# Performance work log

Measured on AMD Instinct MI355X. Metric: run time of the kernel, lower is better.

The kernel has to match this reference:

```python
import jax, jax.numpy as jnp
import numpy as np

VOCAB, HID, L, HEADS, INTER, MAXSEQ, NCLS = 30522, 128, 2, 2, 512, 512, 2
HEAD = HID // HEADS
B, S = 128, 512


def _tlin(x, W, b):
    # TernaryLinear: threshold-quantize W to {-1,0,1} with per-tensor scale,
    # then ordinary linear. delta = 0.7*mean|W|, alpha = mean|W| over kept entries.
    absW = jnp.abs(W)
    delta = 0.7 * jnp.mean(absW)
    mask = (absW > delta).astype(W.dtype)
    alpha = jnp.sum(absW * mask) / jnp.maximum(jnp.sum(mask), 1.0)
    Wq = jnp.sign(W) * mask * alpha  # [out, in]
    return jnp.einsum('...i,oi->...o', x, Wq) + b


def _ln(x, g, b, eps=1e-5):
    m = jnp.mean(x, axis=-1, keepdims=True)
    v = jnp.var(x, axis=-1, keepdims=True)
    return (x - m) * jax.lax.rsqrt(v + eps) * g + b


def setup_inputs() -> dict:
    key = jax.random.key(0)
    ks = iter(jax.random.split(key, 64))
    n = lambda shape, s=0.02: jax.random.normal(next(ks), shape, dtype=jnp.float32) * s
    inp = {
        'input_ids': jax.random.randint(next(ks), (B, S), 0, VOCAB, dtype=jnp.int32).astype(jnp.int64),
        'tok_emb': n((VOCAB, HID)),
        'pos_emb': n((MAXSEQ, HID)),
        'ln_g': jnp.ones((HID,), jnp.float32), 'ln_b': jnp.zeros((HID,), jnp.float32),
        'qw': n((L, HID, HID)), 'qb': jnp.zeros((L, HID), jnp.float32),
        'kw': n((L, HID, HID)), 'kb': jnp.zeros((L, HID), jnp.float32),
        'vw': n((L, HID, HID)), 'vb': jnp.zeros((L, HID), jnp.float32),
        'aow': n((L, HID, HID)), 'aob': jnp.zeros((L, HID), jnp.float32),
        'iw': n((L, INTER, HID)), 'ib': jnp.zeros((L, INTER), jnp.float32),
        'fow': n((L, HID, INTER)), 'fob': jnp.zeros((L, HID), jnp.float32),
        'ln1g': jnp.ones((L, HID), jnp.float32), 'ln1b': jnp.zeros((L, HID), jnp.float32),
        'ln2g': jnp.ones((L, HID), jnp.float32), 'ln2b': jnp.zeros((L, HID), jnp.float32),
        'clf_w': n((NCLS, HID)), 'clf_b': jnp.zeros((NCLS,), jnp.float32),
    }
    return inp


def reference(input_ids, tok_emb, pos_emb, ln_g, ln_b, qw, qb, kw, kb, vw, vb,
              aow, aob, iw, ib, fow, fob, ln1g, ln1b, ln2g, ln2b, clf_w, clf_b):
    b, s = input_ids.shape
    x = tok_emb[input_ids] + pos_emb[jnp.arange(s)][None, :, :]  # [B,S,H]
    x = _ln(x, ln_g, ln_b)
    scale = 1.0 / (HEAD ** 0.5)
    for l in range(L):
        q = _tlin(x, qw[l], qb[l]).reshape(b, s, HEADS, HEAD)
        k = _tlin(x, kw[l], kb[l]).reshape(b, s, HEADS, HEAD)
        v = _tlin(x, vw[l], vb[l]).reshape(b, s, HEADS, HEAD)
        scores = jnp.einsum('bqhd,bkhd->bhqk', q, k) * scale
        attn = jax.nn.softmax(scores, axis=-1)
        ctx = jnp.einsum('bhqk,bkhd->bqhd', attn, v).reshape(b, s, HID)
        attn_out = _tlin(ctx, aow[l], aob[l])
        x = _ln(x + attn_out, ln1g[l], ln1b[l])
        ff = _tlin(jax.nn.relu(_tlin(x, iw[l], ib[l])), fow[l], fob[l])
        x = _ln(x + ff, ln2g[l], ln2b[l])
    cls = x[:, 0, :]
    logits = _tlin(cls, clf_w, clf_b)  # [B, NCLS]
    return logits
```

## Files before the change

kernel.cpp:

```cpp
#include <hip/hip_runtime.h>

typedef short bf8s __attribute__((ext_vector_type(8)));
typedef float f32x4 __attribute__((ext_vector_type(4)));

#define MFMA16(a, b, c) __builtin_amdgcn_mfma_f32_16x16x32_bf16(a, b, c, 0, 0, 0)

constexpr int S_ = 512, HID_ = 128, B_ = 128, M_ = B_ * S_;

__device__ inline short f2bf(float f) {
  unsigned u = __float_as_uint(f);
  u = (u + 0x7fffu + ((u >> 16) & 1u)) >> 16;
  return (short)u;
}
__device__ inline float bf2f(short s) {
  return __uint_as_float(((unsigned)(unsigned short)s) << 16);
}

__device__ __forceinline__ void async16(void* lds, const void* g) {
  __builtin_amdgcn_global_load_lds(
      (const __attribute__((address_space(1))) unsigned int*)g,
      (__attribute__((address_space(3))) unsigned int*)lds, 16, 0, 0);
}

__device__ __forceinline__ bf8s ldsb(const short* base, int byteoff) {
  return *(const bf8s*)((const char*)base + byteoff);
}

__device__ inline float block_red1024(float v, float* red) {
  #pragma unroll
  for (int m = 32; m >= 1; m >>= 1) v += __shfl_xor(v, m);
  __syncthreads();
  if ((threadIdx.x & 63) == 0) red[threadIdx.x >> 6] = v;
  __syncthreads();
  float t = 0.f;
  #pragma unroll
  for (int i = 0; i < 16; ++i) t += red[i];
  return t;
}

__device__ inline void mat_info(int mat, const float* qw, const float* kw,
                                const float* vw, const float* aow, const float* iw,
                                const float* fw, const float* cw,
                                const float** src, int* n, int* doff, int* lc) {
  if (mat < 6) {
    int l = mat / 3, which = mat % 3;
    const float* t[3] = {qw, kw, vw};
    *src = t[which] + l * 16384; *n = 16384; *doff = l * 49152 + which * 16384;
    *lc = 7;
  } else if (mat < 8) {
    int l = mat - 6;
    *src = aow + l * 16384; *n = 16384; *doff = 98304 + l * 16384; *lc = 7;
  } else if (mat < 10) {
    *src = iw + (mat - 8) * 65536; *n = 65536; *doff = 131072 + (mat - 8) * 65536;
    *lc = 7;
  } else if (mat < 12) {
    *src = fw + (mat - 10) * 65536; *n = 65536; *doff = 262144 + (mat - 10) * 65536;
    *lc = 9;
  } else {
    *src = cw; *n = 256; *doff = 393216; *lc = 0;
  }
}

__global__ __launch_bounds__(1024) void k_qe(const float* qw, const float* kw,
    const float* vw, const float* aow, const float* iw, const float* fw,
    const float* cw, short* WQ,
    const int* __restrict__ ids, const float* __restrict__ tok,
    const float* __restrict__ pos, const float* __restrict__ g,
    const float* __restrict__ bb, short* xb) {
  __shared__ float red[16];
  int tid = threadIdx.x;
  if (blockIdx.x < 13) {
    const float* src; int n, doff, lc;
    mat_info(blockIdx.x, qw, kw, vw, aow, iw, fw, cw, &src, &n, &doff, &lc);
    float s = 0.f;
    for (int i = tid; i < n; i += 1024) s += fabsf(src[i]);
    s = block_red1024(s, red);
    float delta = 0.7f * s / (float)n;
    float s2 = 0.f, c2 = 0.f;
    for (int i = tid; i < n; i += 1024) {
      float a = fabsf(src[i]);
      if (a > delta) { s2 += a; c2 += 1.f; }
    }
    s2 = block_red1024(s2, red);
    c2 = block_red1024(c2, red);
    float alpha = s2 / fmaxf(c2, 1.f);
    if (lc) {
      int nf8 = n >> 3;
      for (int fo8 = tid; fo8 < nf8; fo8 += 1024) {
        int fo = fo8 << 3;
        int tile = fo >> (lc + 4);
        int rem = fo & ((16 << lc) - 1);
        int kblk = rem >> 9;
        int rem2 = rem & 511;
        int sub = rem2 >> 7;
        int r16 = (rem2 >> 3) & 15;
        int r = (tile << 4) | r16;
        int cbase = (kblk << 5) | (sub << 3);
        const float* sp = src + ((size_t)r << lc) + cbase;
        float4 w0 = *(const float4*)(sp);
        float4 w1 = *(const float4*)(sp + 4);
        float wv[8] = {w0.x, w0.y, w0.z, w0.w, w1.x, w1.y, w1.z, w1.w};
        bf8s q;
        #pragma unroll
        for (int j = 0; j < 8; ++j) {
          float w = wv[j];
          q[j] = (fabsf(w) > delta) ? f2bf(w > 0.f ? alpha : -alpha) : (short)0;
        }
        *(bf8s*)(WQ + doff + fo) = q;
      }
    } else {
      for (int i = tid; i < n; i += 1024) {
        float w = src[i];
        WQ[doff + i] = (fabsf(w) > delta) ? f2bf(w > 0.f ? alpha : -alpha) : (short)0;
      }
    }
  } else {
    int wave = tid >> 6, lane = tid & 63;
    int half = lane >> 5, l32 = lane & 31;
    int t = (blockIdx.x - 13) * 32 + wave * 2 + half;
    int s = t & (S_ - 1);
    int id = ids[t];
    int d0 = l32 * 4;
    float4 te = *(const float4*)(tok + (size_t)id * HID_ + d0);
    float4 pe = *(const float4*)(pos + (size_t)s * HID_ + d0);
    float e0 = te.x + pe.x, e1 = te.y + pe.y, e2 = te.z + pe.z, e3 = te.w + pe.w;
    float sum = e0 + e1 + e2 + e3;
    float ssq = e0 * e0 + e1 * e1 + e2 * e2 + e3 * e3;
    #pragma unroll
    for (int m = 16; m >= 1; m >>= 1) {
      sum += __shfl_xor(sum, m);
      ssq += __shfl_xor(ssq, m);
    }
    float mean = sum / 128.f;
    float var = ssq / 128.f - mean * mean;
    float rs = rsqrtf(var + 1e-5f);
    float4 g4 = *(const float4*)(g + d0);
    float4 b4 = *(const float4*)(bb + d0);
    short4 o;
    o.x = f2bf((e0 - mean) * rs * g4.x + b4.x);
    o.y = f2bf((e1 - mean) * rs * g4.y + b4.y);
    o.z = f2bf((e2 - mean) * rs * g4.z + b4.z);
    o.w = f2bf((e3 - mean) * rs * g4.w + b4.w);
    *(short4*)(xb + (size_t)t * HID_ + d0) = o;
  }
}

__global__ __launch_bounds__(256) void k_qkv(
    const short* __restrict__ A, const short* __restrict__ W,
    const float* __restrict__ b0, const float* __restrict__ b1,
    const float* __restrict__ b2, short* outb) {
  __shared__ short Wl[16384];
  int tid = threadIdx.x, lane = tid & 63, wave = tid >> 6;
  int row16 = lane & 15, quad = lane >> 4;
  int tok0 = blockIdx.x * 64 + wave * 16;

  const char* Wm = (const char*)W + blockIdx.y * 32768;
  #pragma unroll
  for (int t = 0; t < 8; ++t)
    async16((char*)Wl + t * 4096 + wave * 1024,
            Wm + t * 4096 + wave * 1024 + lane * 16);

  const short* arow = A + (size_t)(tok0 + row16) * 128 + quad * 8;
  bf8s av[4];
  #pragma unroll
  for (int ki = 0; ki < 4; ++ki) av[ki] = *(const bf8s*)(arow + ki * 32);
  __syncthreads();

  f32x4 acc[8] = {};
  #pragma unroll
  for (int ki = 0; ki < 4; ++ki)
    #pragma unroll
    for (int ot = 0; ot < 8; ++ot) {
      bf8s b = ldsb(Wl, ot * 4096 + ki * 1024 + lane * 16);
      acc[ot] = MFMA16(av[ki], b, acc[ot]);
    }

  const float* bp = (blockIdx.y == 0) ? b0 : ((blockIdx.y == 1) ? b1 : b2);
  float osc = (blockIdx.y == 0) ? 0.125f : 1.0f;
  int m0 = tok0 + quad * 4;
  #pragma unroll
  for (int ot = 0; ot < 8; ++ot) {
    int col = ot * 16 + row16;
    float bi = bp[col];
    #pragma unroll
    for (int r = 0; r < 4; ++r) {
      float v = (acc[ot][r] + bi) * osc;
      outb[(size_t)(m0 + r) * 384 + blockIdx.y * 128 + col] = f2bf(v);
    }
  }
}

template <int DOQKV>
__global__ __launch_bounds__(512, 4) void k_aoff(
    const short* __restrict__ cb, const short* __restrict__ Wa,
    const float* __restrict__ aob, const float* __restrict__ ln1g,
    const float* __restrict__ ln1b, const short* __restrict__ Wi,
    const short* __restrict__ Wf, const float* __restrict__ ib,
    const float* __restrict__ fb, const float* __restrict__ ln2g,
    const float* __restrict__ ln2b, short* xb,
    const short* __restrict__ Wqkv2, const float* __restrict__ qb2,
    const float* __restrict__ kb2, const float* __restrict__ vb2,
    short* qkvout) {
  __shared__ short SM[39936];
  int tid = threadIdx.x, lane = tid & 63, wave = tid >> 6;
  int row16 = lane & 15, quad = lane >> 4;
  int tok0 = blockIdx.x * 128 + wave * 16;
  short* mySt = SM + 16384 + wave * 640;
  short* myX  = SM + 21504 + wave * 2304;
  int xr = lane >> 2, xs = (lane & 3) * 32;
  int lb = lane * 16;

  {
    #pragma unroll
    for (int t = 0; t < 4; ++t)
      async16((char*)SM + t * 8192 + wave * 1024,
              (const char*)Wa + t * 8192 + wave * 1024 + lb);
    const short* src = xb + (size_t)(tok0 + xr) * HID_ + xs;
    bf8s x0 = *(const bf8s*)(src);
    bf8s x1 = *(const bf8s*)(src + 8);
    bf8s x2 = *(const bf8s*)(src + 16);
    bf8s x3 = *(const bf8s*)(src + 24);
    short* dst = myX + xr * 144 + xs;
    *(bf8s*)(dst) = x0;      *(bf8s*)(dst + 8) = x1;
    *(bf8s*)(dst + 16) = x2; *(bf8s*)(dst + 24) = x3;
  }

  const short* arow = cb + (size_t)(tok0 + row16) * 128 + quad * 8;
  bf8s av[4];
  #pragma unroll
  for (int ki = 0; ki < 4; ++ki) av[ki] = *(const bf8s*)(arow + ki * 32);
  __syncthreads();

  f32x4 acc[8] = {};
  #pragma unroll
  for (int ki = 0; ki < 4; ++ki)
    #pragma unroll
    for (int ot = 0; ot < 8; ++ot) {
      bf8s b = ldsb(SM, ot * 4096 + ki * 1024 + lb);
      acc[ot] = MFMA16(av[ki], b, acc[ot]);
    }
  __syncthreads();

  {
    async16((char*)SM + wave * 1024, (const char*)Wi + wave * 1024 + lb);
    async16((char*)SM + 16384 + wave * 1024,
            (const char*)Wf + wave * 16384 + lb);
  }

  {
    float sum[4] = {}, ssq[4] = {};
    #pragma unroll
    for (int ot = 0; ot < 8; ++ot) {
      int col = ot * 16 + row16;
      float bi = aob[col];
      #pragma unroll
      for (int r = 0; r < 4; ++r) {
        float v = acc[ot][r] + bi + bf2f(myX[(quad * 4 + r) * 144 + col]);
        acc[ot][r] = v;
        sum[r] += v; ssq[r] += v * v;
      }
    }
    #pragma unroll
    for (int m = 1; m <= 8; m <<= 1)
      #pragma unroll
      for (int r = 0; r < 4; ++r) {
        sum[r] += __shfl_xor(sum[r], m);
        ssq[r] += __shfl_xor(ssq[r], m);
      }
    float mean[4], rstd[4];
    #pragma unroll
    for (int r = 0; r < 4; ++r) {
      mean[r] = sum[r] / 128.f;
      float var = ssq[r] / 128.f - mean[r] * mean[r];
      rstd[r] = rsqrtf(var + 1e-5f);
    }
    #pragma unroll
    for (int ot = 0; ot < 8; ++ot) {
      int col = ot * 16 + row16;
      float gg = ln1g[col], bb2 = ln1b[col];
      #pragma unroll
      for (int r = 0; r < 4; ++r)
        acc[ot][r] = (acc[ot][r] - mean[r]) * rstd[r] * gg + bb2;
    }
  }

  #pragma unroll
  for (int ot = 0; ot < 8; ++ot) {
    int col = ot * 16 + row16;
    #pragma unroll
    for (int r = 0; r < 4; ++r)
      myX[(quad * 4 + r) * 144 + col] = f2bf(acc[ot][r]);
  }
  #pragma unroll
  for (int ki = 0; ki < 4; ++ki)
    av[ki] = *(const bf8s*)(myX + row16 * 144 + ki * 32 + quad * 8);
  __syncthreads();

  f32x4 acc2[8] = {};
  for (int c = 0; c < 16; ++c) {
    int side = c & 1;
    if (c < 15) {
      int cn = c + 1, sn = cn & 1;
      async16((char*)SM + sn * 8192 + wave * 1024,
              (const char*)Wi + cn * 8192 + wave * 1024 + lb);
      async16((char*)SM + 16384 + sn * 8192 + wave * 1024,
              (const char*)Wf + wave * 16384 + cn * 1024 + lb);
    } else if (DOQKV) {
      async16((char*)SM + wave * 1024, (const char*)Wqkv2 + wave * 1024 + lb);
      async16((char*)SM + 16384 + wave * 1024,
              (const char*)Wqkv2 + 8192 + wave * 1024 + lb);
    }

    #pragma unroll
    for (int ot = 0; ot < 2; ++ot) {
      f32x4 hacc = {};
      #pragma unroll
      for (int ki = 0; ki < 4; ++ki) {
        bf8s b = ldsb(SM, side * 8192 + ot * 4096 + ki * 1024 + lb);
        hacc = MFMA16(av[ki], b, hacc);
      }
      float bi = ib[c * 32 + ot * 16 + row16];
      #pragma unroll
      for (int r = 0; r < 4; ++r)
        mySt[(quad * 4 + r) * 40 + ot * 16 + row16] =
            f2bf(fmaxf(hacc[r] + bi, 0.f));
    }
    bf8s ha = *(const bf8s*)(mySt + row16 * 40 + quad * 8);
    #pragma unroll
    for (int ot = 0; ot < 8; ++ot) {
      bf8s bB = ldsb(SM, 16384 + side * 8192 + ot * 1024 + lb);
      acc2[ot] = MFMA16(ha, bB, acc2[ot]);
    }
    __syncthreads();
  }

  {
    float sum[4] = {}, ssq[4] = {};
    #pragma unroll
    for (int ot = 0; ot < 8; ++ot) {
      int col = ot * 16 + row16;
      float bi = fb[col];
      #pragma unroll
      for (int r = 0; r < 4; ++r) {
        float v = acc2[ot][r] + bi + bf2f(myX[(quad * 4 + r) * 144 + col]);
        acc2[ot][r] = v;
        sum[r] += v; ssq[r] += v * v;
      }
    }
    #pragma unroll
    for (int m = 1; m <= 8; m <<= 1)
      #pragma unroll
      for (int r = 0; r < 4; ++r) {
        sum[r] += __shfl_xor(sum[r], m);
        ssq[r] += __shfl_xor(ssq[r], m);
      }
    float mean[4], rstd[4];
    #pragma unroll
    for (int r = 0; r < 4; ++r) {
      mean[r] = sum[r] / 128.f;
      float var = ssq[r] / 128.f - mean[r] * mean[r];
      rstd[r] = rsqrtf(var + 1e-5f);
    }
    #pragma unroll
    for (int ot = 0; ot < 8; ++ot) {
      int col = ot * 16 + row16;
      float gg = ln2g[col], bb2 = ln2b[col];
      #pragma unroll
      for (int r = 0; r < 4; ++r)
        acc2[ot][r] = (acc2[ot][r] - mean[r]) * rstd[r] * gg + bb2;
    }
  }

  #pragma unroll
  for (int ot = 0; ot < 8; ++ot) {
    int col = ot * 16 + row16;
    #pragma unroll
    for (int r = 0; r < 4; ++r)
      myX[(quad * 4 + r) * 144 + col] = f2bf(acc2[ot][r]);
  }
  {
    const short* src = myX + xr * 144 + xs;
    short* dst = xb + (size_t)(tok0 + xr) * HID_ + xs;
    #pragma unroll
    for (int j = 0; j < 4; ++j)
      *(bf8s*)(dst + j * 8) = *(const bf8s*)(src + j * 8);
  }

  if (DOQKV) {
    bf8s av2[4];
    #pragma unroll
    for (int ki = 0; ki < 4; ++ki)
      av2[ki] = *(const bf8s*)(myX + row16 * 144 + ki * 32 + quad * 8);
    for (int j = 0; j < 6; ++j) {
      int side = j & 1;
      if (j < 5) {
        int jn = j + 1, sn = jn & 1;
        async16((char*)SM + sn * 8192 + wave * 1024,
                (const char*)Wqkv2 + jn * 16384 + wave * 1024 + lb);
        async16((char*)SM + 16384 + sn * 8192 + wave * 1024,
                (const char*)Wqkv2 + jn * 16384 + 8192 + wave * 1024 + lb);
      }
      f32x4 acc3[4] = {};
      #pragma unroll
      for (int ki = 0; ki < 4; ++ki)
        #pragma unroll
        for (int ot = 0; ot < 4; ++ot) {
          int bb_ = (ot < 2) ? side * 8192 + ot * 4096
                             : 16384 + side * 8192 + (ot - 2) * 4096;
          bf8s b = ldsb(SM, bb_ + ki * 1024 + lb);
          acc3[ot] = MFMA16(av2[ki], b, acc3[ot]);
        }
      const float* bp = (j < 2) ? qb2 : ((j < 4) ? kb2 : vb2);
      float osc = (j < 2) ? 0.125f : 1.0f;
      #pragma unroll
      for (int ot = 0; ot < 4; ++ot) {
        int col = ot * 16 + row16;
        float bi = bp[(j & 1) * 64 + col];
        #pragma unroll
        for (int r = 0; r < 4; ++r)
          myX[(quad * 4 + r) * 144 + col] = f2bf((acc3[ot][r] + bi) * osc);
      }
      {
        int xr2 = lane >> 2, xs2 = (lane & 3) * 16;
        const short* src = myX + xr2 * 144 + xs2;
        short* dst = qkvout + (size_t)(tok0 + xr2) * 384 + j * 64 + xs2;
        *(bf8s*)(dst) = *(const bf8s*)(src);
        *(bf8s*)(dst + 8) = *(const bf8s*)(src + 8);
      }
      __syncthreads();
    }
  }
}

__global__ __launch_bounds__(512) void k_attn(const short* __restrict__ qkv,
                                              short* __restrict__ O) {
  __shared__ short Kl[64 * 72];
  __shared__ short Vtl[64 * 72];
  __shared__ short Pl[8][16 * 72];

  int tid = threadIdx.x, lane = tid & 63, wave = tid >> 6;
  int row16 = lane & 15, quad = lane >> 4;
  int b = blockIdx.x >> 2, h = (blockIdx.x >> 1) & 1, qhalf = blockIdx.x & 1;
  const short* base  = qkv + (size_t)b * S_ * 384;
  const short* kbase = base + 128 + h * 64;
  const short* vbase = base + 256 + h * 64;
  int q0 = qhalf * 256 + wave * 32;

  bf8s qa[2][2];
  #pragma unroll
  for (int qf = 0; qf < 2; ++qf) {
    const short* qrow = base + h * 64 +
        (size_t)(q0 + qf * 16 + row16) * 384 + quad * 8;
    qa[qf][0] = *(const bf8s*)(qrow);
    qa[qf][1] = *(const bf8s*)(qrow + 32);
  }

  int krow = tid >> 3, dgk = tid & 7;
  int vkey = tid & 63, dgv = tid >> 6;
  const short* kptr = kbase + (size_t)krow * 384 + dgk * 8;
  const short* vptr = vbase + (size_t)vkey * 384 + dgv * 8;
  bf8s kst = *(const bf8s*)(kptr);
  bf8s vst = *(const bf8s*)(vptr);

  float li[2][4] = {};
  f32x4 oacc[2][4] = {};
  short* myP = &Pl[wave][0];

  for (int kt0 = 0; kt0 < S_; kt0 += 64) {
    if (kt0) __syncthreads();
    *(bf8s*)(&Kl[krow * 72 + dgk * 8]) = kst;
    #pragma unroll
    for (int j = 0; j < 8; ++j) Vtl[(dgv * 8 + j) * 72 + vkey] = vst[j];
    __syncthreads();
    if (kt0 + 64 < S_) {
      kst = *(const bf8s*)(kptr + (size_t)(kt0 + 64) * 384);
      vst = *(const bf8s*)(vptr + (size_t)(kt0 + 64) * 384);
    }

    f32x4 sc[2][4] = {};
    #pragma unroll
    for (int ks = 0; ks < 4; ++ks) {
      const short* kp = &Kl[(ks * 16 + row16) * 72 + quad * 8];
      bf8s k0 = *(const bf8s*)(kp);
      bf8s k1 = *(const bf8s*)(kp + 32);
      sc[0][ks] = MFMA16(qa[0][0], k0, sc[0][ks]);
      sc[0][ks] = MFMA16(qa[0][1], k1, sc[0][ks]);
      sc[1][ks] = MFMA16(qa[1][0], k0, sc[1][ks]);
      sc[1][ks] = MFMA16(qa[1][1], k1, sc[1][ks]);
    }

    #pragma unroll
    for (int qf = 0; qf < 2; ++qf) {
      #pragma unroll
      for (int ks = 0; ks < 4; ++ks)
        #pragma unroll
        for (int r = 0; r < 4; ++r) {
          float pv = __expf(sc[qf][ks][r]);
          li[qf][r] += pv;
          myP[(quad * 4 + r) * 72 + ks * 16 + row16] = f2bf(pv);
        }
      bf8s pa0 = *(const bf8s*)(&myP[row16 * 72 + quad * 8]);
      bf8s pa1 = *(const bf8s*)(&myP[row16 * 72 + 32 + quad * 8]);
      #pragma unroll
      for (int dt = 0; dt < 4; ++dt) {
        const short* vp = &Vtl[(dt * 16 + row16) * 72 + quad * 8];
        bf8s v0 = *(const bf8s*)(vp);
        bf8s v1 = *(const bf8s*)(vp + 32);
        oacc[qf][dt] = MFMA16(pa0, v0, oacc[qf][dt]);
        oacc[qf][dt] = MFMA16(pa1, v1, oacc[qf][dt]);
      }
    }
  }

  #pragma unroll
  for (int qf = 0; qf < 2; ++qf) {
    float inv[4];
    #pragma unroll
    for (int r = 0; r < 4; ++r) {
      float t = li[qf][r];
      #pragma unroll
      for (int m = 1; m <= 8; m <<= 1) t += __shfl_xor(t, m);
      inv[r] = 1.f / t;
    }
    size_t trow = (size_t)(b * S_ + q0 + qf * 16 + quad * 4);
    #pragma unroll
    for (int dt = 0; dt < 4; ++dt)
      #pragma unroll
      for (int r = 0; r < 4; ++r)
        O[(trow + r) * HID_ + h * 64 + dt * 16 + row16] =
            f2bf(oacc[qf][dt][r] * inv[r]);
  }
}

__global__ __launch_bounds__(256) void k_clf(const short* __restrict__ xb,
    const short* __restrict__ Wc, const float* __restrict__ cbias, float* out) {
  int i = threadIdx.x;
  int b = i >> 1, c = i & 1;
  float s = 0.f;
  for (int k = 0; k < HID_; ++k)
    s += bf2f(xb[(size_t)b * S_ * HID_ + k]) * bf2f(Wc[c * HID_ + k]);
  out[b * 2 + c] = s + cbias[c];
}

extern "C" void kernel_launch(void* const* d_in, const int* in_sizes, int n_in,
                              void* d_out, int out_size, void* d_ws, size_t ws_size,
                              hipStream_t stream) {
  const int*   ids     = (const int*)d_in[0];
  const float* tok_emb = (const float*)d_in[1];
  const float* pos_emb = (const float*)d_in[2];
  const float* ln_g    = (const float*)d_in[3];
  const float* ln_bb   = (const float*)d_in[4];
  const float* qw      = (const float*)d_in[5];
  const float* qbias   = (const float*)d_in[6];
  const float* kw      = (const float*)d_in[7];
  const float* kbias   = (const float*)d_in[8];
  const float* vw      = (const float*)d_in[9];
  const float* vbias   = (const float*)d_in[10];
  const float* aow     = (const float*)d_in[11];
  const float* aobias  = (const float*)d_in[12];
  const float* iw      = (const float*)d_in[13];
  const float* ibias   = (const float*)d_in[14];
  const float* fow     = (const float*)d_in[15];
  const float* fbias   = (const float*)d_in[16];
  const float* ln1g    = (const float*)d_in[17];
  const float* ln1b    = (const float*)d_in[18];
  const float* ln2g    = (const float*)d_in[19];
  const float* ln2b    = (const float*)d_in[20];
  const float* clfw    = (const float*)d_in[21];
  const float* clfb    = (const float*)d_in[22];

  char* ws = (char*)d_ws;
  short* WQ  = (short*)ws;
  short* xb  = (short*)(ws + 1048576);
  short* qkv = (short*)(ws + 1048576 + 16777216);
  short* cb_ = qkv + (size_t)M_ * 384;

  k_qe<<<13 + M_ / 32, 1024, 0, stream>>>(qw, kw, vw, aow, iw, fow, clfw, WQ,
                                          ids, tok_emb, pos_emb, ln_g, ln_bb, xb);

  const short* Wqkv0 = WQ;
  const short* Wqkv1 = WQ + 49152;
  const short* Wa0   = WQ + 98304;
  const short* Wa1   = WQ + 98304 + 16384;
  const short* Wi0   = WQ + 131072;
  const short* Wi1   = WQ + 131072 + 65536;
  const short* Wf0   = WQ + 262144;
  const short* Wf1   = WQ + 262144 + 65536;

  k_qkv<<<dim3(M_ / 64, 3), 256, 0, stream>>>(
      xb, Wqkv0, qbias, kbias, vbias, qkv);
  k_attn<<<512, 512, 0, stream>>>(qkv, cb_);
  k_aoff<1><<<M_ / 128, 512, 0, stream>>>(
      cb_, Wa0, aobias, ln1g, ln1b, Wi0, Wf0, ibias, fbias, ln2g, ln2b, xb,
      Wqkv1, qbias + HID_, kbias + HID_, vbias + HID_, qkv);
  k_attn<<<512, 512, 0, stream>>>(qkv, cb_);
  k_aoff<0><<<M_ / 128, 512, 0, stream>>>(
      cb_, Wa1, aobias + HID_, ln1g + HID_, ln1b + HID_, Wi1, Wf1,
      ibias + 512, fbias + HID_, ln2g + HID_, ln2b + HID_, xb,
      nullptr, nullptr, nullptr, nullptr, nullptr);

  k_clf<<<1, 256, 0, stream>>>(xb, WQ + 393216, clfb, (float*)d_out);
}
```

Measured before the change: 306.5 us.

## Restructure fused attn-out/FFN kernel to 32-token wave tiles with split columns

```diff
diff --git a/kernel.cpp b/kernel.cpp
--- a/kernel.cpp
+++ b/kernel.cpp
@@ -174,24 +174,31 @@
       bf8s b = ldsb(Wl, ot * 4096 + ki * 1024 + lane * 16);
       acc[ot] = MFMA16(av[ki], b, acc[ot]);
     }
+  __syncthreads();
 
   const float* bp = (blockIdx.y == 0) ? b0 : ((blockIdx.y == 1) ? b1 : b2);
   float osc = (blockIdx.y == 0) ? 0.125f : 1.0f;
-  int m0 = tok0 + quad * 4;
+  short* scr = Wl + wave * 2112;
   #pragma unroll
   for (int ot = 0; ot < 8; ++ot) {
     int col = ot * 16 + row16;
     float bi = bp[col];
     #pragma unroll
-    for (int r = 0; r < 4; ++r) {
-      float v = (acc[ot][r] + bi) * osc;
-      outb[(size_t)(m0 + r) * 384 + blockIdx.y * 128 + col] = f2bf(v);
-    }
+    for (int r = 0; r < 4; ++r)
+      scr[(quad * 4 + r) * 132 + col] = f2bf((acc[ot][r] + bi) * osc);
+  }
+  {
+    int rr = lane >> 2, cg = lane & 3;
+    const short* src = scr + rr * 132 + cg * 32;
+    short* dst = outb + (size_t)(tok0 + rr) * 384 + blockIdx.y * 128 + cg * 32;
+    #pragma unroll
+    for (int j = 0; j < 4; ++j)
+      *(bf8s*)(dst + j * 8) = *(const bf8s*)(src + j * 8);
   }
 }
 
 template <int DOQKV>
-__global__ __launch_bounds__(512, 4) void k_aoff(
+__global__ __launch_bounds__(256, 3) void k_aoff(
     const short* __restrict__ cb, const short* __restrict__ Wa,
     const float* __restrict__ aob, const float* __restrict__ ln1g,
     const float* __restrict__ ln1b, const short* __restrict__ Wi,
@@ -201,231 +208,297 @@
     const short* __restrict__ Wqkv2, const float* __restrict__ qb2,
     const float* __restrict__ kb2, const float* __restrict__ vb2,
     short* qkvout) {
-  __shared__ short SM[39936];
+  __shared__ char SMc[53760];
+  short* SM = (short*)SMc;
+  float* LNred = (float*)(SMc + 8192);
   int tid = threadIdx.x, lane = tid & 63, wave = tid >> 6;
+  int tg = wave >> 1, ch = wave & 1;
   int row16 = lane & 15, quad = lane >> 4;
-  int tok0 = blockIdx.x * 128 + wave * 16;
-  short* mySt = SM + 16384 + wave * 640;
-  short* myX  = SM + 21504 + wave * 2304;
-  int xr = lane >> 2, xs = (lane & 3) * 32;
-  int lb = lane * 16;
-
+  int btok = blockIdx.x * 64;
+  int tok0 = btok + tg * 32;
+  char* myX = SMc + 36864 + tg * 8448;
+  char* stash = SMc + 32768 + tg * 2048;
+
+  #pragma unroll
+  for (int t = 0; t < 8; ++t)
+    async16(SMc + (wave * 8 + t) * 1024,
+            (const char*)Wa + (wave * 8 + t) * 1024 + lane * 16);
   {
-    #pragma unroll
-    for (int t = 0; t < 4; ++t)
-      async16((char*)SM + t * 8192 + wave * 1024,
-              (const char*)Wa + t * 8192 + wave * 1024 + lb);
-    const short* src = xb + (size_t)(tok0 + xr) * HID_ + xs;
+    int rr = tid >> 2, cg = tid & 3;
+    const short* src = xb + (size_t)(btok + rr) * HID_ + cg * 32;
     bf8s x0 = *(const bf8s*)(src);
     bf8s x1 = *(const bf8s*)(src + 8);
     bf8s x2 = *(const bf8s*)(src + 16);
     bf8s x3 = *(const bf8s*)(src + 24);
-    short* dst = myX + xr * 144 + xs;
-    *(bf8s*)(dst) = x0;      *(bf8s*)(dst + 8) = x1;
-    *(bf8s*)(dst + 16) = x2; *(bf8s*)(dst + 24) = x3;
-  }
-
-  const short* arow = cb + (size_t)(tok0 + row16) * 128 + quad * 8;
-  bf8s av[4];
-  #pragma unroll
-  for (int ki = 0; ki < 4; ++ki) av[ki] = *(const bf8s*)(arow + ki * 32);
-  __syncthreads();
-
-  f32x4 acc[8] = {};
+    char* dst = SMc + 36864 + (rr >> 5) * 8448 + (rr & 31) * 264 + cg * 64;
+    *(bf8s*)(dst) = x0;      *(bf8s*)(dst + 16) = x1;
+    *(bf8s*)(dst + 32) = x2; *(bf8s*)(dst + 48) = x3;
+  }
+  bf8s av[2][4];
+  #pragma unroll
+  for (int g = 0; g < 2; ++g)
+    #pragma unroll
+    for (int ki = 0; ki < 4; ++ki)
+      av[g][ki] = *(const bf8s*)(cb + (size_t)(tok0 + g * 16 + row16) * 128 +
+                                 ki * 32 + quad * 8);
+  __syncthreads();
+
+  f32x4 acc[2][4] = {};
   #pragma unroll
   for (int ki = 0; ki < 4; ++ki)
     #pragma unroll
-    for (int ot = 0; ot < 8; ++ot) {
-      bf8s b = ldsb(SM, ot * 4096 + ki * 1024 + lb);
-      acc[ot] = MFMA16(av[ki], b, acc[ot]);
+    for (int t = 0; t < 4; ++t) {
+      bf8s b = ldsb(SM, (ch * 4 + t) * 4096 + ki * 1024 + lane * 16);
+      acc[0][t] = MFMA16(av[0][ki], b, acc[0][t]);
+      acc[1][t] = MFMA16(av[1][ki], b, acc[1][t]);
     }
   __syncthreads();
 
   {
-    async16((char*)SM + wave * 1024, (const char*)Wi + wave * 1024 + lb);
-    async16((char*)SM + 16384 + wave * 1024,
-            (const char*)Wf + wave * 16384 + lb);
+    int idx = wave * 2;
+    async16(SMc + idx * 1024, (const char*)Wi + idx * 1024 + lane * 16);
+    async16(SMc + (idx + 1) * 1024, (const char*)Wi + (idx + 1) * 1024 + lane * 16);
+    async16(SMc + 16384 + idx * 1024, (const char*)Wf + idx * 16384 + lane * 16);
+    async16(SMc + 16384 + (idx + 1) * 1024,
+            (const char*)Wf + (idx + 1) * 16384 + lane * 16);
   }
 
   {
-    float sum[4] = {}, ssq[4] = {};
-    #pragma unroll
-    for (int ot = 0; ot < 8; ++ot) {
-      int col = ot * 16 + row16;
-      float bi = aob[col];
+    float sum[2][4] = {}, ssq[2][4] = {};
+    #pragma unroll
+    for (int g = 0; g < 2; ++g)
+      #pragma unroll
+      for (int t = 0; t < 4; ++t) {
+        int col = ch * 64 + t * 16 + row16;
+        float bi = aob[col];
+        #pragma unroll
+        for (int r = 0; r < 4; ++r) {
+          float v = acc[g][t][r] + bi +
+                    bf2f(*(const short*)(myX + (g * 16 + quad * 4 + r) * 264 + col * 2));
+          acc[g][t][r] = v;
+          sum[g][r] += v; ssq[g][r] += v * v;
+        }
+      }
+    #pragma unroll
+    for (int m = 1; m <= 8; m <<= 1)
+      #pragma unroll
+      for (int g = 0; g < 2; ++g)
+        #pragma unroll
+        for (int r = 0; r < 4; ++r) {
+          sum[g][r] += __shfl_xor(sum[g][r], m);
+          ssq[g][r] += __shfl_xor(ssq[g][r], m);
+        }
+    if (row16 == 0) {
+      #pragma unroll
+      for (int g = 0; g < 2; ++g)
+        #pragma unroll
+        for (int r = 0; r < 4; ++r) {
+          int row = g * 16 + quad * 4 + r;
+          LNred[(tg * 64 + ch * 32 + row) * 2] = sum[g][r];
+          LNred[(tg * 64 + ch * 32 + row) * 2 + 1] = ssq[g][r];
+        }
+    }
+    __syncthreads();
+    float mean[2][4], rstd[2][4];
+    #pragma unroll
+    for (int g = 0; g < 2; ++g)
       #pragma unroll
       for (int r = 0; r < 4; ++r) {
-        float v = acc[ot][r] + bi + bf2f(myX[(quad * 4 + r) * 144 + col]);
-        acc[ot][r] = v;
-        sum[r] += v; ssq[r] += v * v;
-      }
-    }
-    #pragma unroll
-    for (int m = 1; m <= 8; m <<= 1)
-      #pragma unroll
-      for (int r = 0; r < 4; ++r) {
-        sum[r] += __shfl_xor(sum[r], m);
-        ssq[r] += __shfl_xor(ssq[r], m);
-      }
-    float mean[4], rstd[4];
-    #pragma unroll
-    for (int r = 0; r < 4; ++r) {
-      mean[r] = sum[r] / 128.f;
-      float var = ssq[r] / 128.f - mean[r] * mean[r];
-      rstd[r] = rsqrtf(var + 1e-5f);
-    }
-    #pragma unroll
-    for (int ot = 0; ot < 8; ++ot) {
-      int col = ot * 16 + row16;
-      float gg = ln1g[col], bb2 = ln1b[col];
-      #pragma unroll
-      for (int r = 0; r < 4; ++r)
-        acc[ot][r] = (acc[ot][r] - mean[r]) * rstd[r] * gg + bb2;
-    }
-  }
-
-  #pragma unroll
-  for (int ot = 0; ot < 8; ++ot) {
-    int col = ot * 16 + row16;
-    #pragma unroll
-    for (int r = 0; r < 4; ++r)
-      myX[(quad * 4 + r) * 144 + col] = f2bf(acc[ot][r]);
-  }
-  #pragma unroll
-  for (int ki = 0; ki < 4; ++ki)
-    av[ki] = *(const bf8s*)(myX + row16 * 144 + ki * 32 + quad * 8);
-  __syncthreads();
-
-  f32x4 acc2[8] = {};
+        int row = g * 16 + quad * 4 + r;
+        float2 p0 = *(const float2*)(LNred + (tg * 64 + row) * 2);
+        float2 p1 = *(const float2*)(LNred + (tg * 64 + 32 + row) * 2);
+        float s = p0.x + p1.x, q = p0.y + p1.y;
+        mean[g][r] = s / 128.f;
+        float var = q / 128.f - mean[g][r] * mean[g][r];
+        rstd[g][r] = rsqrtf(var + 1e-5f);
+      }
+    #pragma unroll
+    for (int g = 0; g < 2; ++g)
+      #pragma unroll
+      for (int t = 0; t < 4; ++t) {
+        int col = ch * 64 + t * 16 + row16;
+        float gg = ln1g[col], bb2 = ln1b[col];
+        #pragma unroll
+        for (int r = 0; r < 4; ++r) {
+          float v = (acc[g][t][r] - mean[g][r]) * rstd[g][r] * gg + bb2;
+          *(short*)(myX + (g * 16 + quad * 4 + r) * 264 + col * 2) = f2bf(v);
+        }
+      }
+  }
+  __syncthreads();
+  #pragma unroll
+  for (int g = 0; g < 2; ++g)
+    #pragma unroll
+    for (int ki = 0; ki < 4; ++ki)
+      av[g][ki] = *(const bf8s*)(myX + (g * 16 + row16) * 264 + ki * 64 + quad * 16);
+
+  f32x4 acc2[2][4] = {};
   for (int c = 0; c < 16; ++c) {
     int side = c & 1;
     if (c < 15) {
-      int cn = c + 1, sn = cn & 1;
-      async16((char*)SM + sn * 8192 + wave * 1024,
-              (const char*)Wi + cn * 8192 + wave * 1024 + lb);
-      async16((char*)SM + 16384 + sn * 8192 + wave * 1024,
-              (const char*)Wf + wave * 16384 + cn * 1024 + lb);
+      int cn = c + 1, sn = cn & 1, idx = wave * 2;
+      async16(SMc + sn * 8192 + idx * 1024,
+              (const char*)Wi + cn * 8192 + idx * 1024 + lane * 16);
+      async16(SMc + sn * 8192 + (idx + 1) * 1024,
+              (const char*)Wi + cn * 8192 + (idx + 1) * 1024 + lane * 16);
+      async16(SMc + 16384 + sn * 8192 + idx * 1024,
+              (const char*)Wf + idx * 16384 + cn * 1024 + lane * 16);
+      async16(SMc + 16384 + sn * 8192 + (idx + 1) * 1024,
+              (const char*)Wf + (idx + 1) * 16384 + cn * 1024 + lane * 16);
     } else if (DOQKV) {
-      async16((char*)SM + wave * 1024, (const char*)Wqkv2 + wave * 1024 + lb);
-      async16((char*)SM + 16384 + wave * 1024,
-              (const char*)Wqkv2 + 8192 + wave * 1024 + lb);
-    }
-
-    #pragma unroll
-    for (int ot = 0; ot < 2; ++ot) {
-      f32x4 hacc = {};
-      #pragma unroll
-      for (int ki = 0; ki < 4; ++ki) {
-        bf8s b = ldsb(SM, side * 8192 + ot * 4096 + ki * 1024 + lb);
-        hacc = MFMA16(av[ki], b, hacc);
-      }
-      float bi = ib[c * 32 + ot * 16 + row16];
-      #pragma unroll
-      for (int r = 0; r < 4; ++r)
-        mySt[(quad * 4 + r) * 40 + ot * 16 + row16] =
-            f2bf(fmaxf(hacc[r] + bi, 0.f));
-    }
-    bf8s ha = *(const bf8s*)(mySt + row16 * 40 + quad * 8);
-    #pragma unroll
-    for (int ot = 0; ot < 8; ++ot) {
-      bf8s bB = ldsb(SM, 16384 + side * 8192 + ot * 1024 + lb);
-      acc2[ot] = MFMA16(ha, bB, acc2[ot]);
+      #pragma unroll
+      for (int sub = 0; sub < 4; ++sub)
+        async16(SMc + (wave >> 1) * 16384 + (wave & 1) * 4096 + sub * 1024,
+                (const char*)Wqkv2 + wave * 4096 + sub * 1024 + lane * 16);
+    }
+    f32x4 h0 = {}, h1 = {};
+    #pragma unroll
+    for (int ki = 0; ki < 4; ++ki) {
+      bf8s b = ldsb(SM, side * 8192 + ch * 4096 + ki * 1024 + lane * 16);
+      h0 = MFMA16(av[0][ki], b, h0);
+      h1 = MFMA16(av[1][ki], b, h1);
+    }
+    float bi = ib[c * 32 + ch * 16 + row16];
+    #pragma unroll
+    for (int r = 0; r < 4; ++r) {
+      *(short*)(stash + (quad * 4 + r) * 64 + (ch * 16 + row16) * 2) =
+          f2bf(fmaxf(h0[r] + bi, 0.f));
+      *(short*)(stash + (16 + quad * 4 + r) * 64 + (ch * 16 + row16) * 2) =
+          f2bf(fmaxf(h1[r] + bi, 0.f));
     }
     __syncthreads();
+    bf8s ha0 = *(const bf8s*)(stash + row16 * 64 + quad * 16);
+    bf8s ha1 = *(const bf8s*)(stash + (16 + row16) * 64 + quad * 16);
+    #pragma unroll
+    for (int t = 0; t < 4; ++t) {
+      bf8s bB = ldsb(SM, 16384 + side * 8192 + (ch * 4 + t) * 1024 + lane * 16);
+      acc2[0][t] = MFMA16(ha0, bB, acc2[0][t]);
+      acc2[1][t] = MFMA16(ha1, bB, acc2[1][t]);
+    }
+    __syncthreads();
   }
 
   {
-    float sum[4] = {}, ssq[4] = {};
-    #pragma unroll
-    for (int ot = 0; ot < 8; ++ot) {
-      int col = ot * 16 + row16;
-      float bi = fb[col];
+    float sum[2][4] = {}, ssq[2][4] = {};
+    #pragma unroll
+    for (int g = 0; g < 2; ++g)
+      #pragma unroll
+      for (int t = 0; t < 4; ++t) {
+        int col = ch * 64 + t * 16 + row16;
+        float bi = fb[col];
+        #pragma unroll
+        for (int r = 0; r < 4; ++r) {
+          float v = acc2[g][t][r] + bi +
+                    bf2f(*(const short*)(myX + (g * 16 + quad * 4 + r) * 264 + col * 2));
+          acc2[g][t][r] = v;
+          sum[g][r] += v; ssq[g][r] += v * v;
+        }
+      }
+    #pragma unroll
+    for (int m = 1; m <= 8; m <<= 1)
+      #pragma unroll
+      for (int g = 0; g < 2; ++g)
+        #pragma unroll
+        for (int r = 0; r < 4; ++r) {
+          sum[g][r] += __shfl_xor(sum[g][r], m);
+          ssq[g][r] += __shfl_xor(ssq[g][r], m);
+        }
+    if (row16 == 0) {
+      #pragma unroll
+      for (int g = 0; g < 2; ++g)
+        #pragma unroll
+        for (int r = 0; r < 4; ++r) {
+          int row = g * 16 + quad * 4 + r;
+          LNred[(tg * 64 + ch * 32 + row) * 2] = sum[g][r];
+          LNred[(tg * 64 + ch * 32 + row) * 2 + 1] = ssq[g][r];
+        }
+    }
+    __syncthreads();
+    float mean[2][4], rstd[2][4];
+    #pragma unroll
+    for (int g = 0; g < 2; ++g)
       #pragma unroll
       for (int r = 0; r < 4; ++r) {
-        float v = acc2[ot][r] + bi + bf2f(myX[(quad * 4 + r) * 144 + col]);
-        acc2[ot][r] = v;
-        sum[r] += v; ssq[r] += v * v;
-      }
-    }
-    #pragma unroll
-    for (int m = 1; m <= 8; m <<= 1)
-      #pragma unroll
-      for (int r = 0; r < 4; ++r) {
-        sum[r] += __shfl_xor(sum[r], m);
-        ssq[r] += __shfl_xor(ssq[r], m);
-      }
-    float mean[4], rstd[4];
-    #pragma unroll
-    for (int r = 0; r < 4; ++r) {
-      mean[r] = sum[r] / 128.f;
-      float var = ssq[r] / 128.f - mean[r] * mean[r];
-      rstd[r] = rsqrtf(var + 1e-5f);
-    }
-    #pragma unroll
-    for (int ot = 0; ot < 8; ++ot) {
-      int col = ot * 16 + row16;
-      float gg = ln2g[col], bb2 = ln2b[col];
-      #pragma unroll
-      for (int r = 0; r < 4; ++r)
-        acc2[ot][r] = (acc2[ot][r] - mean[r]) * rstd[r] * gg + bb2;
-    }
-  }
-
-  #pragma unroll
-  for (int ot = 0; ot < 8; ++ot) {
-    int col = ot * 16 + row16;
-    #pragma unroll
-    for (int r = 0; r < 4; ++r)
-      myX[(quad * 4 + r) * 144 + col] = f2bf(acc2[ot][r]);
-  }
+        int row = g * 16 + quad * 4 + r;
+        float2 p0 = *(const float2*)(LNred + (tg * 64 + row) * 2);
+        float2 p1 = *(const float2*)(LNred + (tg * 64 + 32 + row) * 2);
+        float s = p0.x + p1.x, q = p0.y + p1.y;
+        mean[g][r] = s / 128.f;
+        float var = q / 128.f - mean[g][r] * mean[g][r];
+        rstd[g][r] = rsqrtf(var + 1e-5f);
+      }
+    #pragma unroll
+    for (int g = 0; g < 2; ++g)
+      #pragma unroll
+      for (int t = 0; t < 4; ++t) {
+        int col = ch * 64 + t * 16 + row16;
+        float gg = ln2g[col], bb2 = ln2b[col];
+        #pragma unroll
+        for (int r = 0; r < 4; ++r) {
+          float v = (acc2[g][t][r] - mean[g][r]) * rstd[g][r] * gg + bb2;
+          *(short*)(myX + (g * 16 + quad * 4 + r) * 264 + col * 2) = f2bf(v);
+        }
+      }
+  }
+  __syncthreads();
   {
-    const short* src = myX + xr * 144 + xs;
-    short* dst = xb + (size_t)(tok0 + xr) * HID_ + xs;
-    #pragma unroll
-    for (int j = 0; j < 4; ++j)
-      *(bf8s*)(dst + j * 8) = *(const bf8s*)(src + j * 8);
+    int rr = tid >> 2, cg = tid & 3;
+    const char* src = SMc + 36864 + (rr >> 5) * 8448 + (rr & 31) * 264 + cg * 64;
+    short* dst = xb + (size_t)(btok + rr) * HID_ + cg * 32;
+    *(bf8s*)(dst) = *(const bf8s*)(src);
+    *(bf8s*)(dst + 8) = *(const bf8s*)(src + 16);
+    *(bf8s*)(dst + 16) = *(const bf8s*)(src + 32);
+    *(bf8s*)(dst + 24) = *(const bf8s*)(src + 48);
   }
 
   if (DOQKV) {
-    bf8s av2[4];
-    #pragma unroll
-    for (int ki = 0; ki < 4; ++ki)
-      av2[ki] = *(const bf8s*)(myX + row16 * 144 + ki * 32 + quad * 8);
+    bf8s av2[2][4];
+    #pragma unroll
+    for (int g = 0; g < 2; ++g)
+      #pragma unroll
+      for (int ki = 0; ki < 4; ++ki)
+        av2[g][ki] = *(const bf8s*)(myX + (g * 16 + row16) * 264 + ki * 64 + quad * 16);
     for (int j = 0; j < 6; ++j) {
       int side = j & 1;
       if (j < 5) {
         int jn = j + 1, sn = jn & 1;
-        async16((char*)SM + sn * 8192 + wave * 1024,
-                (const char*)Wqkv2 + jn * 16384 + wave * 1024 + lb);
-        async16((char*)SM + 16384 + sn * 8192 + wave * 1024,
-                (const char*)Wqkv2 + jn * 16384 + 8192 + wave * 1024 + lb);
-      }
-      f32x4 acc3[4] = {};
+        #pragma unroll
+        for (int sub = 0; sub < 4; ++sub)
+          async16(SMc + (wave >> 1) * 16384 + sn * 8192 + (wave & 1) * 4096 + sub * 1024,
+                  (const char*)Wqkv2 + jn * 16384 + wave * 4096 + sub * 1024 + lane * 16);
+      }
+      f32x4 a3[2][2] = {};
       #pragma unroll
       for (int ki = 0; ki < 4; ++ki)
         #pragma unroll
-        for (int ot = 0; ot < 4; ++ot) {
-          int bb_ = (ot < 2) ? side * 8192 + ot * 4096
-                             : 16384 + side * 8192 + (ot - 2) * 4096;
-          bf8s b = ldsb(SM, bb_ + ki * 1024 + lb);
-          acc3[ot] = MFMA16(av2[ki], b, acc3[ot]);
-        }
-      const float* bp = (j < 2) ? qb2 : ((j < 4) ? kb2 : vb2);
-      float osc = (j < 2) ? 0.125f : 1.0f;
-      #pragma unroll
-      for (int ot = 0; ot < 4; ++ot) {
-        int col = ot * 16 + row16;
-        float bi = bp[(j & 1) * 64 + col];
-        #pragma unroll
-        for (int r = 0; r < 4; ++r)
-          myX[(quad * 4 + r) * 144 + col] = f2bf((acc3[ot][r] + bi) * osc);
+        for (int t = 0; t < 2; ++t) {
+          int t4 = ch * 2 + t;
+          bf8s b = ldsb(SM, (t4 >> 1) * 16384 + side * 8192 + (t4 & 1) * 4096 +
+                                ki * 1024 + lane * 16);
+          a3[0][t] = MFMA16(av2[0][ki], b, a3[0][t]);
+          a3[1][t] = MFMA16(av2[1][ki], b, a3[1][t]);
+        }
+      int colbase = j * 64 + ch * 32;
+      int mat = colbase >> 7;
+      const float* bp = (mat == 0) ? qb2 : ((mat == 1) ? kb2 : vb2);
+      float osc = (mat == 0) ? 0.125f : 1.0f;
+      #pragma unroll
+      for (int t = 0; t < 2; ++t) {
+        int lcol = ch * 32 + t * 16 + row16;
+        float bi = bp[(colbase + t * 16 + row16) & 127];
+        #pragma unroll
+        for (int g = 0; g < 2; ++g)
+          #pragma unroll
+          for (int r = 0; r < 4; ++r)
+            *(short*)(myX + (g * 16 + quad * 4 + r) * 264 + lcol * 2) =
+                f2bf((a3[g][t][r] + bi) * osc);
       }
       {
-        int xr2 = lane >> 2, xs2 = (lane & 3) * 16;
-        const short* src = myX + xr2 * 144 + xs2;
-        short* dst = qkvout + (size_t)(tok0 + xr2) * 384 + j * 64 + xs2;
+        int rrow = lane >> 1, hf = lane & 1;
+        const char* src = myX + rrow * 264 + (ch * 32 + hf * 16) * 2;
+        short* dst = qkvout + (size_t)(tok0 + rrow) * 384 + j * 64 + ch * 32 + hf * 16;
         *(bf8s*)(dst) = *(const bf8s*)(src);
-        *(bf8s*)(dst + 8) = *(const bf8s*)(src + 8);
+        *(bf8s*)(dst + 8) = *(const bf8s*)(src + 16);
       }
       __syncthreads();
     }
@@ -590,11 +663,11 @@
   k_qkv<<<dim3(M_ / 64, 3), 256, 0, stream>>>(
       xb, Wqkv0, qbias, kbias, vbias, qkv);
   k_attn<<<512, 512, 0, stream>>>(qkv, cb_);
-  k_aoff<1><<<M_ / 128, 512, 0, stream>>>(
+  k_aoff<1><<<M_ / 64, 256, 0, stream>>>(
       cb_, Wa0, aobias, ln1g, ln1b, Wi0, Wf0, ibias, fbias, ln2g, ln2b, xb,
       Wqkv1, qbias + HID_, kbias + HID_, vbias + HID_, qkv);
   k_attn<<<512, 512, 0, stream>>>(qkv, cb_);
-  k_aoff<0><<<M_ / 128, 512, 0, stream>>>(
+  k_aoff<0><<<M_ / 64, 256, 0, stream>>>(
       cb_, Wa1, aobias + HID_, ln1g + HID_, ln1b + HID_, Wi1, Wf1,
       ibias + 512, fbias + HID_, ln2g + HID_, ln2b + HID_, xb,
       nullptr, nullptr, nullptr, nullptr, nullptr);
```

Result: slower. 353.4 us (+15.3%).

## Split attention into quarter-query blocks and stage QKV output through LDS

Applied to the files above, without the earlier changes.

```diff
diff --git a/kernel.cpp b/kernel.cpp
--- a/kernel.cpp
+++ b/kernel.cpp
@@ -174,19 +174,26 @@
       bf8s b = ldsb(Wl, ot * 4096 + ki * 1024 + lane * 16);
       acc[ot] = MFMA16(av[ki], b, acc[ot]);
     }
+  __syncthreads();
 
   const float* bp = (blockIdx.y == 0) ? b0 : ((blockIdx.y == 1) ? b1 : b2);
   float osc = (blockIdx.y == 0) ? 0.125f : 1.0f;
-  int m0 = tok0 + quad * 4;
+  short* scr = Wl + wave * 2112;
   #pragma unroll
   for (int ot = 0; ot < 8; ++ot) {
     int col = ot * 16 + row16;
     float bi = bp[col];
     #pragma unroll
-    for (int r = 0; r < 4; ++r) {
-      float v = (acc[ot][r] + bi) * osc;
-      outb[(size_t)(m0 + r) * 384 + blockIdx.y * 128 + col] = f2bf(v);
-    }
+    for (int r = 0; r < 4; ++r)
+      scr[(quad * 4 + r) * 132 + col] = f2bf((acc[ot][r] + bi) * osc);
+  }
+  {
+    int rr = lane >> 2, cg = lane & 3;
+    const short* src = scr + rr * 132 + cg * 32;
+    short* dst = outb + (size_t)(tok0 + rr) * 384 + blockIdx.y * 128 + cg * 32;
+    #pragma unroll
+    for (int j = 0; j < 4; ++j)
+      *(bf8s*)(dst + j * 8) = *(const bf8s*)(src + j * 8);
   }
 }
 
@@ -440,19 +447,20 @@
 
   int tid = threadIdx.x, lane = tid & 63, wave = tid >> 6;
   int row16 = lane & 15, quad = lane >> 4;
-  int b = blockIdx.x >> 2, h = (blockIdx.x >> 1) & 1, qhalf = blockIdx.x & 1;
+  int idx = blockIdx.x;
+  int qq = (idx >> 3) & 3;
+  int bh = ((idx >> 5) << 3) | (idx & 7);
+  int b = bh >> 1, h = bh & 1;
   const short* base  = qkv + (size_t)b * S_ * 384;
   const short* kbase = base + 128 + h * 64;
   const short* vbase = base + 256 + h * 64;
-  int q0 = qhalf * 256 + wave * 32;
-
-  bf8s qa[2][2];
-  #pragma unroll
-  for (int qf = 0; qf < 2; ++qf) {
-    const short* qrow = base + h * 64 +
-        (size_t)(q0 + qf * 16 + row16) * 384 + quad * 8;
-    qa[qf][0] = *(const bf8s*)(qrow);
-    qa[qf][1] = *(const bf8s*)(qrow + 32);
+  int q0 = qq * 128 + wave * 16;
+
+  bf8s qa0, qa1;
+  {
+    const short* qrow = base + h * 64 + (size_t)(q0 + row16) * 384 + quad * 8;
+    qa0 = *(const bf8s*)(qrow);
+    qa1 = *(const bf8s*)(qrow + 32);
   }
 
   int krow = tid >> 3, dgk = tid & 7;
@@ -462,8 +470,8 @@
   bf8s kst = *(const bf8s*)(kptr);
   bf8s vst = *(const bf8s*)(vptr);
 
-  float li[2][4] = {};
-  f32x4 oacc[2][4] = {};
+  float li[4] = {};
+  f32x4 oacc[4] = {};
   short* myP = &Pl[wave][0];
 
   for (int kt0 = 0; kt0 < S_; kt0 += 64) {
@@ -477,59 +485,51 @@
       vst = *(const bf8s*)(vptr + (size_t)(kt0 + 64) * 384);
     }
 
-    f32x4 sc[2][4] = {};
+    f32x4 sc[4] = {};
     #pragma unroll
     for (int ks = 0; ks < 4; ++ks) {
       const short* kp = &Kl[(ks * 16 + row16) * 72 + quad * 8];
       bf8s k0 = *(const bf8s*)(kp);
       bf8s k1 = *(const bf8s*)(kp + 32);
-      sc[0][ks] = MFMA16(qa[0][0], k0, sc[0][ks]);
-      sc[0][ks] = MFMA16(qa[0][1], k1, sc[0][ks]);
-      sc[1][ks] = MFMA16(qa[1][0], k0, sc[1][ks]);
-      sc[1][ks] = MFMA16(qa[1][1], k1, sc[1][ks]);
-    }
-
-    #pragma unroll
-    for (int qf = 0; qf < 2; ++qf) {
-      #pragma unroll
-      for (int ks = 0; ks < 4; ++ks)
-        #pragma unroll
-        for (int r = 0; r < 4; ++r) {
-          float pv = __expf(sc[qf][ks][r]);
-          li[qf][r] += pv;
-          myP[(quad * 4 + r) * 72 + ks * 16 + row16] = f2bf(pv);
-        }
-      bf8s pa0 = *(const bf8s*)(&myP[row16 * 72 + quad * 8]);
-      bf8s pa1 = *(const bf8s*)(&myP[row16 * 72 + 32 + quad * 8]);
-      #pragma unroll
-      for (int dt = 0; dt < 4; ++dt) {
-        const short* vp = &Vtl[(dt * 16 + row16) * 72 + quad * 8];
-        bf8s v0 = *(const bf8s*)(vp);
-        bf8s v1 = *(const bf8s*)(vp + 32);
-        oacc[qf][dt] = MFMA16(pa0, v0, oacc[qf][dt]);
-        oacc[qf][dt] = MFMA16(pa1, v1, oacc[qf][dt]);
-      }
-    }
-  }
-
-  #pragma unroll
-  for (int qf = 0; qf < 2; ++qf) {
-    float inv[4];
-    #pragma unroll
-    for (int r = 0; r < 4; ++r) {
-      float t = li[qf][r];
-      #pragma unroll
-      for (int m = 1; m <= 8; m <<= 1) t += __shfl_xor(t, m);
-      inv[r] = 1.f / t;
-    }
-    size_t trow = (size_t)(b * S_ + q0 + qf * 16 + quad * 4);
-    #pragma unroll
-    for (int dt = 0; dt < 4; ++dt)
-      #pragma unroll
-      for (int r = 0; r < 4; ++r)
-        O[(trow + r) * HID_ + h * 64 + dt * 16 + row16] =
-            f2bf(oacc[qf][dt][r] * inv[r]);
-  }
+      sc[ks] = MFMA16(qa0, k0, sc[ks]);
+      sc[ks] = MFMA16(qa1, k1, sc[ks]);
+    }
+
+    #pragma unroll
+    for (int ks = 0; ks < 4; ++ks)
+      #pragma unroll
+      for (int r = 0; r < 4; ++r) {
+        float pv = __expf(sc[ks][r]);
+        li[r] += pv;
+        myP[(quad * 4 + r) * 72 + ks * 16 + row16] = f2bf(pv);
+      }
+    bf8s pa0 = *(const bf8s*)(&myP[row16 * 72 + quad * 8]);
+    bf8s pa1 = *(const bf8s*)(&myP[row16 * 72 + 32 + quad * 8]);
+    #pragma unroll
+    for (int dt = 0; dt < 4; ++dt) {
+      const short* vp = &Vtl[(dt * 16 + row16) * 72 + quad * 8];
+      bf8s v0 = *(const bf8s*)(vp);
+      bf8s v1 = *(const bf8s*)(vp + 32);
+      oacc[dt] = MFMA16(pa0, v0, oacc[dt]);
+      oacc[dt] = MFMA16(pa1, v1, oacc[dt]);
+    }
+  }
+
+  float inv[4];
+  #pragma unroll
+  for (int r = 0; r < 4; ++r) {
+    float t = li[r];
+    #pragma unroll
+    for (int m = 1; m <= 8; m <<= 1) t += __shfl_xor(t, m);
+    inv[r] = 1.f / t;
+  }
+  size_t trow = (size_t)(b * S_ + q0 + quad * 4);
+  #pragma unroll
+  for (int dt = 0; dt < 4; ++dt)
+    #pragma unroll
+    for (int r = 0; r < 4; ++r)
+      O[(trow + r) * HID_ + h * 64 + dt * 16 + row16] =
+          f2bf(oacc[dt][r] * inv[r]);
 }
 
 __global__ __launch_bounds__(256) void k_clf(const short* __restrict__ xb,
@@ -589,11 +589,11 @@
 
   k_qkv<<<dim3(M_ / 64, 3), 256, 0, stream>>>(
       xb, Wqkv0, qbias, kbias, vbias, qkv);
-  k_attn<<<512, 512, 0, stream>>>(qkv, cb_);
+  k_attn<<<1024, 512, 0, stream>>>(qkv, cb_);
   k_aoff<1><<<M_ / 128, 512, 0, stream>>>(
       cb_, Wa0, aobias, ln1g, ln1b, Wi0, Wf0, ibias, fbias, ln2g, ln2b, xb,
       Wqkv1, qbias + HID_, kbias + HID_, vbias + HID_, qkv);
-  k_attn<<<512, 512, 0, stream>>>(qkv, cb_);
+  k_attn<<<1024, 512, 0, stream>>>(qkv, cb_);
   k_aoff<0><<<M_ / 128, 512, 0, stream>>>(
       cb_, Wa1, aobias + HID_, ln1g + HID_, ln1b + HID_, Wi1, Wf1,
       ibias + 512, fbias + HID_, ln2g + HID_, ln2b + HID_, xb,
```

Result: slower. 321.7 us (+5.0%).
